# Optimization experiments

Hardware: AMD Instinct MI355X
Metric: run time of the kernel (lower is better)

Reference implementation:

```python
import jax, jax.numpy as jnp
import numpy as np

N_EMBD = 1024
BLOCK_SIZE = 2048
ATTN_SPAN = 256
LN_EPS = 1e-5


def _band_mask(T, span, dtype):
    ones = jnp.ones((T, T), dtype=dtype)
    # tril(.,0) * (1 - tril(.,-span)) -> causal band of width `span`
    return jnp.tril(ones, 0) * (1.0 - jnp.tril(ones, -span))


def setup_inputs() -> dict:
    key = jax.random.key(0)
    k_x, k_w, k_b, k_lw = jax.random.split(key, 4)
    B, T, C = 4, BLOCK_SIZE, N_EMBD
    x = jax.random.normal(k_x, (B, T, C), dtype=jnp.float32)
    # qkv_net: Linear(C, 3C) with bias (torch default)
    lim = 1.0 / np.sqrt(C)
    W_qkv = jax.random.uniform(k_w, (C, 3 * C), minval=-lim, maxval=lim, dtype=jnp.float32)
    b_qkv = jax.random.uniform(k_b, (3 * C,), minval=-lim, maxval=lim, dtype=jnp.float32)
    ln_w = jnp.ones((C,), dtype=jnp.float32)
    ln_b = jnp.zeros((C,), dtype=jnp.float32)
    return {"x": x, "W_qkv": W_qkv, "b_qkv": b_qkv, "ln_w": ln_w, "ln_b": ln_b}


def _layer_norm(h, w, b):
    mu = jnp.mean(h, axis=-1, keepdims=True)
    var = jnp.var(h, axis=-1, keepdims=True)
    return (h - mu) * jax.lax.rsqrt(var + LN_EPS) * w + b


def reference(x, W_qkv, b_qkv, ln_w, ln_b):
    B, T, C = x.shape
    qkv = x @ W_qkv + b_qkv  # [B,T,3C]
    q, k, v = jnp.split(qkv, 3, axis=-1)
    scale = np.sqrt(C * ATTN_SPAN).astype(np.float32)
    scores = jnp.einsum('bid,bjd->bij', q, k) / scale  # [B,T,T]
    scores = scores * _band_mask(T, ATTN_SPAN, x.dtype)[None, :, :]
    out = jnp.einsum('bij,bjd->bid', scores, v)  # [B,T,C]
    return _layer_norm(out, ln_w, ln_b)
```

## Files before the change

### kernel.cpp

```cpp
#include <hip/hip_runtime.h>
#include <cstdint>
#include <cstddef>

#define N_EMBD 1024
#define T_SEQ  2048
#define NBATCH 4
#define SPAN   256
#define C3     3072

typedef float  floatx4 __attribute__((ext_vector_type(4)));
typedef __bf16 bf16x8  __attribute__((ext_vector_type(8)));

__device__ inline unsigned short f2bf(float f) {
    union { float f; unsigned u; } x; x.f = f;
    unsigned u = x.u;
    unsigned r = (u + 0x7fffu + ((u >> 16) & 1u)) >> 16;
    return (unsigned short)r;
}

typedef __attribute__((address_space(1))) const void GVOID;
typedef __attribute__((address_space(3))) void LVOID;
__device__ inline void gl2lds16(const void* g, void* l) {
    __builtin_amdgcn_global_load_lds((GVOID*)g, (LVOID*)l, 16, 0, 0);
}

__global__ __launch_bounds__(256) void k_cvt_x(const float* __restrict__ x,
                                               unsigned short* __restrict__ xb) {
    int i = (blockIdx.x * 256 + threadIdx.x) * 4;
    float4 v = *(const float4*)(x + i);
    ushort4 o;
    o.x = f2bf(v.x); o.y = f2bf(v.y); o.z = f2bf(v.z); o.w = f2bf(v.w);
    *(ushort4*)(xb + i) = o;
}

__global__ __launch_bounds__(256) void k_cvt_w_t(const float* __restrict__ W,
                                                 unsigned short* __restrict__ WbT) {
    __shared__ unsigned short t[32][33];
    int tx = threadIdx.x & 31, ty = threadIdx.x >> 5;
    int k0 = blockIdx.x * 32, n0 = blockIdx.y * 32;
#pragma unroll
    for (int i = 0; i < 4; i++) {
        int k = k0 + ty + i * 8;
        t[ty + i * 8][tx] = f2bf(W[(size_t)k * C3 + n0 + tx]);
    }
    __syncthreads();
#pragma unroll
    for (int i = 0; i < 4; i++) {
        int n = n0 + ty + i * 8;
        WbT[(size_t)n * N_EMBD + k0 + tx] = t[tx][ty + i * 8];
    }
}

__global__ __launch_bounds__(256) void k_qkv_gemm(const unsigned short* __restrict__ Xb,
                                                  const unsigned short* __restrict__ WbT,
                                                  const float* __restrict__ bqkv,
                                                  unsigned short* __restrict__ qkv) {
    __shared__ unsigned short As[128 * 32];
    __shared__ unsigned short Bs[128 * 32];
    const int tid = threadIdx.x, lane = tid & 63, wave = tid >> 6;
    const int n0 = blockIdx.x * 128, m0 = blockIdx.y * 128;
    const int wr = wave >> 1, wc = wave & 1;

    floatx4 acc[4][4] = {};

    const int srow = wave * 16 + (lane >> 2);
    const int scol = (lane & 3) * 8;
    const unsigned short* gA = Xb  + (size_t)(m0 + srow) * N_EMBD + scol;
    const unsigned short* gB = WbT + (size_t)(n0 + srow) * N_EMBD + scol;

    for (int k0 = 0; k0 < N_EMBD; k0 += 32) {
        gl2lds16(gA + k0,              &As[(wave * 16) * 32]);
        gl2lds16(gA + 64 * N_EMBD + k0, &As[(64 + wave * 16) * 32]);
        gl2lds16(gB + k0,              &Bs[(wave * 16) * 32]);
        gl2lds16(gB + 64 * N_EMBD + k0, &Bs[(64 + wave * 16) * 32]);
        __syncthreads();

        bf16x8 a[4], b[4];
        const int qk = (lane >> 4) * 8;
        const int ra = wr * 64 + (lane & 15);
        const int rb = wc * 64 + (lane & 15);
#pragma unroll
        for (int mi = 0; mi < 4; mi++) a[mi] = *(const bf16x8*)&As[(ra + mi * 16) * 32 + qk];
#pragma unroll
        for (int ni = 0; ni < 4; ni++) b[ni] = *(const bf16x8*)&Bs[(rb + ni * 16) * 32 + qk];
#pragma unroll
        for (int mi = 0; mi < 4; mi++)
#pragma unroll
            for (int ni = 0; ni < 4; ni++)
                acc[mi][ni] = __builtin_amdgcn_mfma_f32_16x16x32_bf16(a[mi], b[ni], acc[mi][ni], 0, 0, 0);
        __syncthreads();
    }

    const int cn = lane & 15, q = lane >> 4;
#pragma unroll
    for (int ni = 0; ni < 4; ni++) {
        const int n = n0 + wc * 64 + ni * 16 + cn;
        const float bias = bqkv[n];
#pragma unroll
        for (int mi = 0; mi < 4; mi++) {
            const int mbase = m0 + wr * 64 + mi * 16 + q * 4;
#pragma unroll
            for (int r = 0; r < 4; r++)
                qkv[(size_t)(mbase + r) * C3 + n] = f2bf(acc[mi][ni][r] + bias);
        }
    }
}

__global__ __launch_bounds__(256) void k_v_t(const unsigned short* __restrict__ qkv,
                                             unsigned short* __restrict__ Vt) {
    __shared__ unsigned short t[32][33];
    int tx = threadIdx.x & 31, ty = threadIdx.x >> 5;
    int t0 = blockIdx.x * 32, c0 = blockIdx.y * 32, b = blockIdx.z;
#pragma unroll
    for (int i = 0; i < 4; i++) {
        int tt = t0 + ty + i * 8;
        t[ty + i * 8][tx] = qkv[(size_t)(b * T_SEQ + tt) * C3 + 2048 + c0 + tx];
    }
    __syncthreads();
#pragma unroll
    for (int i = 0; i < 4; i++) {
        int c = c0 + ty + i * 8;
        Vt[(size_t)b * N_EMBD * T_SEQ + (size_t)c * T_SEQ + t0 + tx] = t[tx][ty + i * 8];
    }
}

__global__ __launch_bounds__(256) void k_scores(const unsigned short* __restrict__ qkv,
                                                unsigned short* __restrict__ S) {
    const int jj = blockIdx.x, qb = blockIdx.y, b = blockIdx.z;
    const int jb = qb - 4 + jj;
    if (jb < 0) return;

    __shared__ unsigned short Qs[64 * 64];
    __shared__ unsigned short Ks[64 * 64];
    const int tid = threadIdx.x, lane = tid & 63, wave = tid >> 6;
    const int wr = wave >> 1, wc = wave & 1;

    floatx4 acc[2][2] = {};

    const int srow = wave * 8 + (lane >> 3);
    const int scol = (lane & 7) * 8;
    const unsigned short* gQ = qkv + (size_t)(b * T_SEQ + qb * 64 + srow) * C3 + scol;
    const unsigned short* gK = qkv + (size_t)(b * T_SEQ + jb * 64 + srow) * C3 + 1024 + scol;

    for (int k0 = 0; k0 < N_EMBD; k0 += 64) {
        gl2lds16(gQ + k0,                   &Qs[(wave * 8) * 64]);
        gl2lds16(gQ + (size_t)32 * C3 + k0, &Qs[(32 + wave * 8) * 64]);
        gl2lds16(gK + k0,                   &Ks[(wave * 8) * 64]);
        gl2lds16(gK + (size_t)32 * C3 + k0, &Ks[(32 + wave * 8) * 64]);
        __syncthreads();
#pragma unroll
        for (int ks = 0; ks < 2; ks++) {
            bf16x8 a[2], bb[2];
            const int qk = ks * 32 + (lane >> 4) * 8;
#pragma unroll
            for (int mi = 0; mi < 2; mi++) a[mi]  = *(const bf16x8*)&Qs[(wr * 32 + mi * 16 + (lane & 15)) * 64 + qk];
#pragma unroll
            for (int ni = 0; ni < 2; ni++) bb[ni] = *(const bf16x8*)&Ks[(wc * 32 + ni * 16 + (lane & 15)) * 64 + qk];
#pragma unroll
            for (int mi = 0; mi < 2; mi++)
#pragma unroll
                for (int ni = 0; ni < 2; ni++)
                    acc[mi][ni] = __builtin_amdgcn_mfma_f32_16x16x32_bf16(a[mi], bb[ni], acc[mi][ni], 0, 0, 0);
        }
        __syncthreads();
    }

    unsigned short* Sb = S + (((size_t)(b * 32 + qb) * 5 + jj) << 12);
    const int cn = lane & 15, q = lane >> 4;
#pragma unroll
    for (int mi = 0; mi < 2; mi++)
#pragma unroll
        for (int ni = 0; ni < 2; ni++)
#pragma unroll
            for (int r = 0; r < 4; r++) {
                const int il = wr * 32 + mi * 16 + q * 4 + r;
                const int jl = wc * 32 + ni * 16 + cn;
                const int gi = qb * 64 + il, gj = jb * 64 + jl;
                const float v = ((gj <= gi) && (gj > gi - 256)) ? acc[mi][ni][r] * (1.0f / 512.0f) : 0.0f;
                Sb[il * 64 + jl] = f2bf(v);
            }
}

__global__ __launch_bounds__(256) void k_sv(const unsigned short* __restrict__ S,
                                            const unsigned short* __restrict__ Vt,
                                            float* __restrict__ out) {
    const int cg = blockIdx.x, qb = blockIdx.y, b = blockIdx.z;
    const int c0 = cg * 128;

    __shared__ unsigned short Ss[64 * 64];
    __shared__ unsigned short Vs[128 * 64];
    const int tid = threadIdx.x, lane = tid & 63, wave = tid >> 6;
    const int wr = wave >> 1, wc = wave & 1;

    floatx4 acc[2][4] = {};

    const int srow = wave * 8 + (lane >> 3);
    const int scol = (lane & 7) * 8;

    for (int jj = 0; jj < 5; jj++) {
        const int jb = qb - 4 + jj;
        if (jb < 0) continue;

        const unsigned short* gS = S + (((size_t)(b * 32 + qb) * 5 + jj) << 12) + srow * 64 + scol;
        gl2lds16(gS,           &Ss[(wave * 8) * 64]);
        gl2lds16(gS + 32 * 64, &Ss[(32 + wave * 8) * 64]);
        const unsigned short* gV = Vt + (size_t)b * N_EMBD * T_SEQ
                                      + (size_t)(c0 + srow) * T_SEQ + jb * 64 + scol;
#pragma unroll
        for (int is = 0; is < 4; is++)
            gl2lds16(gV + (size_t)is * 32 * T_SEQ, &Vs[(is * 32 + wave * 8) * 64]);
        __syncthreads();
#pragma unroll
        for (int ks = 0; ks < 2; ks++) {
            bf16x8 a[2], bb[4];
            const int qk = ks * 32 + (lane >> 4) * 8;
#pragma unroll
            for (int mi = 0; mi < 2; mi++) a[mi]  = *(const bf16x8*)&Ss[(wr * 32 + mi * 16 + (lane & 15)) * 64 + qk];
#pragma unroll
            for (int ni = 0; ni < 4; ni++) bb[ni] = *(const bf16x8*)&Vs[(wc * 64 + ni * 16 + (lane & 15)) * 64 + qk];
#pragma unroll
            for (int mi = 0; mi < 2; mi++)
#pragma unroll
                for (int ni = 0; ni < 4; ni++)
                    acc[mi][ni] = __builtin_amdgcn_mfma_f32_16x16x32_bf16(a[mi], bb[ni], acc[mi][ni], 0, 0, 0);
        }
        __syncthreads();
    }

    const int cn = lane & 15, q = lane >> 4;
#pragma unroll
    for (int mi = 0; mi < 2; mi++)
#pragma unroll
        for (int ni = 0; ni < 4; ni++)
#pragma unroll
            for (int r = 0; r < 4; r++) {
                const int il = wr * 32 + mi * 16 + q * 4 + r;
                const int cl = wc * 64 + ni * 16 + cn;
                out[(size_t)(b * T_SEQ + qb * 64 + il) * N_EMBD + c0 + cl] = acc[mi][ni][r];
            }
}

__global__ __launch_bounds__(256) void k_ln(float* __restrict__ out,
                                            const float* __restrict__ w,
                                            const float* __restrict__ bias) {
    __shared__ float red[8];
    const int t = threadIdx.x;
    float* p = out + (size_t)blockIdx.x * N_EMBD;
    float4 v = ((const float4*)p)[t];
    float s  = v.x + v.y + v.z + v.w;
    float sq = v.x * v.x + v.y * v.y + v.z * v.z + v.w * v.w;
#pragma unroll
    for (int off = 32; off; off >>= 1) {
        s  += __shfl_down(s, off, 64);
        sq += __shfl_down(sq, off, 64);
    }
    const int wave = t >> 6, lane = t & 63;
    if (lane == 0) { red[wave] = s; red[4 + wave] = sq; }
    __syncthreads();
    const float ts = red[0] + red[1] + red[2] + red[3];
    const float tq = red[4] + red[5] + red[6] + red[7];
    const float mean = ts * (1.0f / N_EMBD);
    const float var  = tq * (1.0f / N_EMBD) - mean * mean;
    const float rs = rsqrtf(var + 1e-5f);
    float4 wv = ((const float4*)w)[t];
    float4 bv = ((const float4*)bias)[t];
    float4 o;
    o.x = (v.x - mean) * rs * wv.x + bv.x;
    o.y = (v.y - mean) * rs * wv.y + bv.y;
    o.z = (v.z - mean) * rs * wv.z + bv.z;
    o.w = (v.w - mean) * rs * wv.w + bv.w;
    ((float4*)p)[t] = o;
}

extern "C" void kernel_launch(void* const* d_in, const int* in_sizes, int n_in,
                              void* d_out, int out_size, void* d_ws, size_t ws_size,
                              hipStream_t stream) {
    const float* x  = (const float*)d_in[0];
    const float* W  = (const float*)d_in[1];
    const float* bq = (const float*)d_in[2];
    const float* lw = (const float*)d_in[3];
    const float* lb = (const float*)d_in[4];
    float* out = (float*)d_out;
    char* ws = (char*)d_ws;

    unsigned short* Xb   = (unsigned short*)(ws + 0);
    unsigned short* Sbuf = (unsigned short*)(ws + 0);
    unsigned short* WbT  = (unsigned short*)(ws + 16777216);
    unsigned short* qkv  = (unsigned short*)(ws + 23068672);
    unsigned short* Vt   = (unsigned short*)(ws + 73400320);

    k_cvt_x   <<<8192,            256, 0, stream>>>(x, Xb);
    k_cvt_w_t <<<dim3(32, 96),    256, 0, stream>>>(W, WbT);
    k_qkv_gemm<<<dim3(24, 64),    256, 0, stream>>>(Xb, WbT, bq, qkv);
    k_v_t     <<<dim3(64, 32, 4), 256, 0, stream>>>(qkv, Vt);
    k_scores  <<<dim3(5, 32, 4),  256, 0, stream>>>(qkv, Sbuf);
    k_sv      <<<dim3(8, 32, 4),  256, 0, stream>>>(Sbuf, Vt, out);
    k_ln      <<<8192,            256, 0, stream>>>(out, lw, lb);
}
```

Measured before the change: 213.5 us.

## Fuse conversion kernels, transpose V in GEMM epilogue, use 128-row attention tiles

The x and W bf16 conversions become a single launch. The V transpose moves into the QKV GEMM epilogue through an LDS staging tile, which removes the separate transpose kernel and the extra qkv round trip. Q and K are stored packed. The score and SV kernels switch from 64-row to 128-row tiles with 3 key blocks instead of 5, and LDS loads use an XOR-swizzled layout to avoid bank conflicts. This cuts launches, redundant band work and memory traffic, at the cost of fewer blocks in the attention kernels, which may lower occupancy.

```diff
diff --git a/kernel.cpp b/kernel.cpp
--- a/kernel.cpp
+++ b/kernel.cpp
@@ -24,61 +24,69 @@
     __builtin_amdgcn_global_load_lds((GVOID*)g, (LVOID*)l, 16, 0, 0);
 }
 
-__global__ __launch_bounds__(256) void k_cvt_x(const float* __restrict__ x,
-                                               unsigned short* __restrict__ xb) {
-    int i = (blockIdx.x * 256 + threadIdx.x) * 4;
-    float4 v = *(const float4*)(x + i);
-    ushort4 o;
-    o.x = f2bf(v.x); o.y = f2bf(v.y); o.z = f2bf(v.z); o.w = f2bf(v.w);
-    *(ushort4*)(xb + i) = o;
-}
-
-__global__ __launch_bounds__(256) void k_cvt_w_t(const float* __restrict__ W,
-                                                 unsigned short* __restrict__ WbT) {
+__device__ inline void stage128x32(const unsigned short* g, size_t stride,
+                                   unsigned short* lds, int lane, int wave) {
+    const int r     = wave * 16 + (lane >> 2);
+    const int chunk = (lane & 3) ^ ((lane >> 3) & 3);
+    const unsigned short* src = g + (size_t)r * stride + chunk * 8;
+    gl2lds16(src,               &lds[(wave * 16) * 32]);
+    gl2lds16(src + 64 * stride, &lds[(64 + wave * 16) * 32]);
+}
+
+__global__ __launch_bounds__(256) void k_prep(const float* __restrict__ x,
+                                              unsigned short* __restrict__ Xb,
+                                              const float* __restrict__ W,
+                                              unsigned short* __restrict__ WbT) {
     __shared__ unsigned short t[32][33];
-    int tx = threadIdx.x & 31, ty = threadIdx.x >> 5;
-    int k0 = blockIdx.x * 32, n0 = blockIdx.y * 32;
-#pragma unroll
-    for (int i = 0; i < 4; i++) {
-        int k = k0 + ty + i * 8;
-        t[ty + i * 8][tx] = f2bf(W[(size_t)k * C3 + n0 + tx]);
-    }
-    __syncthreads();
-#pragma unroll
-    for (int i = 0; i < 4; i++) {
-        int n = n0 + ty + i * 8;
-        WbT[(size_t)n * N_EMBD + k0 + tx] = t[tx][ty + i * 8];
+    if (blockIdx.x < 8192) {
+        int i = (blockIdx.x * 256 + threadIdx.x) * 4;
+        float4 v = *(const float4*)(x + i);
+        ushort4 o;
+        o.x = f2bf(v.x); o.y = f2bf(v.y); o.z = f2bf(v.z); o.w = f2bf(v.w);
+        *(ushort4*)(Xb + i) = o;
+    } else {
+        int bid = blockIdx.x - 8192;
+        int k0 = (bid & 31) * 32, n0 = (bid >> 5) * 32;
+        int tx = threadIdx.x & 31, ty = threadIdx.x >> 5;
+#pragma unroll
+        for (int i = 0; i < 4; i++) {
+            int k = k0 + ty + i * 8;
+            t[ty + i * 8][tx] = f2bf(W[(size_t)k * C3 + n0 + tx]);
+        }
+        __syncthreads();
+#pragma unroll
+        for (int i = 0; i < 4; i++) {
+            int n = n0 + ty + i * 8;
+            WbT[(size_t)n * N_EMBD + k0 + tx] = t[tx][ty + i * 8];
+        }
     }
 }
 
 __global__ __launch_bounds__(256) void k_qkv_gemm(const unsigned short* __restrict__ Xb,
                                                   const unsigned short* __restrict__ WbT,
                                                   const float* __restrict__ bqkv,
-                                                  unsigned short* __restrict__ qkv) {
-    __shared__ unsigned short As[128 * 32];
-    __shared__ unsigned short Bs[128 * 32];
+                                                  unsigned short* __restrict__ QK,
+                                                  unsigned short* __restrict__ Vt) {
+    __shared__ unsigned short smem[17408];
+    unsigned short* As = smem;
+    unsigned short* Bs = smem + 4096;
     const int tid = threadIdx.x, lane = tid & 63, wave = tid >> 6;
     const int n0 = blockIdx.x * 128, m0 = blockIdx.y * 128;
     const int wr = wave >> 1, wc = wave & 1;
 
     floatx4 acc[4][4] = {};
 
-    const int srow = wave * 16 + (lane >> 2);
-    const int scol = (lane & 3) * 8;
-    const unsigned short* gA = Xb  + (size_t)(m0 + srow) * N_EMBD + scol;
-    const unsigned short* gB = WbT + (size_t)(n0 + srow) * N_EMBD + scol;
+    const unsigned short* gA = Xb  + (size_t)m0 * N_EMBD;
+    const unsigned short* gB = WbT + (size_t)n0 * N_EMBD;
+    const int qk = ((lane >> 4) ^ ((lane >> 1) & 3)) * 8;
+    const int ra = wr * 64 + (lane & 15);
+    const int rb = wc * 64 + (lane & 15);
 
     for (int k0 = 0; k0 < N_EMBD; k0 += 32) {
-        gl2lds16(gA + k0,              &As[(wave * 16) * 32]);
-        gl2lds16(gA + 64 * N_EMBD + k0, &As[(64 + wave * 16) * 32]);
-        gl2lds16(gB + k0,              &Bs[(wave * 16) * 32]);
-        gl2lds16(gB + 64 * N_EMBD + k0, &Bs[(64 + wave * 16) * 32]);
-        __syncthreads();
-
+        stage128x32(gA + k0, N_EMBD, As, lane, wave);
+        stage128x32(gB + k0, N_EMBD, Bs, lane, wave);
+        __syncthreads();
         bf16x8 a[4], b[4];
-        const int qk = (lane >> 4) * 8;
-        const int ra = wr * 64 + (lane & 15);
-        const int rb = wc * 64 + (lane & 15);
 #pragma unroll
         for (int mi = 0; mi < 4; mi++) a[mi] = *(const bf16x8*)&As[(ra + mi * 16) * 32 + qk];
 #pragma unroll
@@ -92,92 +100,95 @@
     }
 
     const int cn = lane & 15, q = lane >> 4;
-#pragma unroll
-    for (int ni = 0; ni < 4; ni++) {
-        const int n = n0 + wc * 64 + ni * 16 + cn;
-        const float bias = bqkv[n];
-#pragma unroll
-        for (int mi = 0; mi < 4; mi++) {
-            const int mbase = m0 + wr * 64 + mi * 16 + q * 4;
-#pragma unroll
-            for (int r = 0; r < 4; r++)
-                qkv[(size_t)(mbase + r) * C3 + n] = f2bf(acc[mi][ni][r] + bias);
-        }
-    }
-}
-
-__global__ __launch_bounds__(256) void k_v_t(const unsigned short* __restrict__ qkv,
-                                             unsigned short* __restrict__ Vt) {
-    __shared__ unsigned short t[32][33];
-    int tx = threadIdx.x & 31, ty = threadIdx.x >> 5;
-    int t0 = blockIdx.x * 32, c0 = blockIdx.y * 32, b = blockIdx.z;
-#pragma unroll
-    for (int i = 0; i < 4; i++) {
-        int tt = t0 + ty + i * 8;
-        t[ty + i * 8][tx] = qkv[(size_t)(b * T_SEQ + tt) * C3 + 2048 + c0 + tx];
-    }
-    __syncthreads();
-#pragma unroll
-    for (int i = 0; i < 4; i++) {
-        int c = c0 + ty + i * 8;
-        Vt[(size_t)b * N_EMBD * T_SEQ + (size_t)c * T_SEQ + t0 + tx] = t[tx][ty + i * 8];
-    }
-}
-
-__global__ __launch_bounds__(256) void k_scores(const unsigned short* __restrict__ qkv,
+    if (n0 < 2048) {
+#pragma unroll
+        for (int ni = 0; ni < 4; ni++) {
+            const int n = n0 + wc * 64 + ni * 16 + cn;
+            const float bias = bqkv[n];
+#pragma unroll
+            for (int mi = 0; mi < 4; mi++) {
+                const int mbase = m0 + wr * 64 + mi * 16 + q * 4;
+#pragma unroll
+                for (int r = 0; r < 4; r++)
+                    QK[(size_t)(mbase + r) * 2048 + n] = f2bf(acc[mi][ni][r] + bias);
+            }
+        }
+    } else {
+        unsigned short* tp = smem;
+#pragma unroll
+        for (int ni = 0; ni < 4; ni++) {
+            const int cl = wc * 64 + ni * 16 + cn;
+            const float bias = bqkv[n0 + cl];
+#pragma unroll
+            for (int mi = 0; mi < 4; mi++) {
+                const int tl = wr * 64 + mi * 16 + q * 4;
+#pragma unroll
+                for (int r = 0; r < 4; r++)
+                    tp[cl * 136 + tl + r] = f2bf(acc[mi][ni][r] + bias);
+            }
+        }
+        __syncthreads();
+        const int clw = tid >> 1, half = tid & 1;
+        const int b = m0 >> 11, tg = (m0 & 2047) + half * 64;
+        const int cg = n0 - 2048 + clw;
+        unsigned short* dst = Vt + ((size_t)(b * 1024 + cg)) * 2048 + tg;
+        const unsigned short* src = tp + clw * 136 + half * 64;
+#pragma unroll
+        for (int i = 0; i < 8; i++)
+            *(uint4*)(dst + i * 8) = *(const uint4*)(src + i * 8);
+    }
+}
+
+__global__ __launch_bounds__(256) void k_scores(const unsigned short* __restrict__ QK,
                                                 unsigned short* __restrict__ S) {
     const int jj = blockIdx.x, qb = blockIdx.y, b = blockIdx.z;
-    const int jb = qb - 4 + jj;
+    const int jb = qb - 2 + jj;
     if (jb < 0) return;
 
-    __shared__ unsigned short Qs[64 * 64];
-    __shared__ unsigned short Ks[64 * 64];
+    __shared__ unsigned short smem[8192];
+    unsigned short* As = smem;
+    unsigned short* Bs = smem + 4096;
     const int tid = threadIdx.x, lane = tid & 63, wave = tid >> 6;
     const int wr = wave >> 1, wc = wave & 1;
 
-    floatx4 acc[2][2] = {};
-
-    const int srow = wave * 8 + (lane >> 3);
-    const int scol = (lane & 7) * 8;
-    const unsigned short* gQ = qkv + (size_t)(b * T_SEQ + qb * 64 + srow) * C3 + scol;
-    const unsigned short* gK = qkv + (size_t)(b * T_SEQ + jb * 64 + srow) * C3 + 1024 + scol;
-
-    for (int k0 = 0; k0 < N_EMBD; k0 += 64) {
-        gl2lds16(gQ + k0,                   &Qs[(wave * 8) * 64]);
-        gl2lds16(gQ + (size_t)32 * C3 + k0, &Qs[(32 + wave * 8) * 64]);
-        gl2lds16(gK + k0,                   &Ks[(wave * 8) * 64]);
-        gl2lds16(gK + (size_t)32 * C3 + k0, &Ks[(32 + wave * 8) * 64]);
-        __syncthreads();
-#pragma unroll
-        for (int ks = 0; ks < 2; ks++) {
-            bf16x8 a[2], bb[2];
-            const int qk = ks * 32 + (lane >> 4) * 8;
-#pragma unroll
-            for (int mi = 0; mi < 2; mi++) a[mi]  = *(const bf16x8*)&Qs[(wr * 32 + mi * 16 + (lane & 15)) * 64 + qk];
-#pragma unroll
-            for (int ni = 0; ni < 2; ni++) bb[ni] = *(const bf16x8*)&Ks[(wc * 32 + ni * 16 + (lane & 15)) * 64 + qk];
-#pragma unroll
-            for (int mi = 0; mi < 2; mi++)
-#pragma unroll
-                for (int ni = 0; ni < 2; ni++)
-                    acc[mi][ni] = __builtin_amdgcn_mfma_f32_16x16x32_bf16(a[mi], bb[ni], acc[mi][ni], 0, 0, 0);
-        }
-        __syncthreads();
-    }
-
-    unsigned short* Sb = S + (((size_t)(b * 32 + qb) * 5 + jj) << 12);
+    floatx4 acc[4][4] = {};
+
+    const unsigned short* gQ = QK + ((size_t)(b * T_SEQ + qb * 128)) * 2048;
+    const unsigned short* gK = QK + ((size_t)(b * T_SEQ + jb * 128)) * 2048 + 1024;
+    const int qk = ((lane >> 4) ^ ((lane >> 1) & 3)) * 8;
+    const int ra = wr * 64 + (lane & 15);
+    const int rb = wc * 64 + (lane & 15);
+
+    for (int k0 = 0; k0 < N_EMBD; k0 += 32) {
+        stage128x32(gQ + k0, 2048, As, lane, wave);
+        stage128x32(gK + k0, 2048, Bs, lane, wave);
+        __syncthreads();
+        bf16x8 a[4], bb[4];
+#pragma unroll
+        for (int mi = 0; mi < 4; mi++) a[mi]  = *(const bf16x8*)&As[(ra + mi * 16) * 32 + qk];
+#pragma unroll
+        for (int ni = 0; ni < 4; ni++) bb[ni] = *(const bf16x8*)&Bs[(rb + ni * 16) * 32 + qk];
+#pragma unroll
+        for (int mi = 0; mi < 4; mi++)
+#pragma unroll
+            for (int ni = 0; ni < 4; ni++)
+                acc[mi][ni] = __builtin_amdgcn_mfma_f32_16x16x32_bf16(a[mi], bb[ni], acc[mi][ni], 0, 0, 0);
+        __syncthreads();
+    }
+
+    unsigned short* Sb = S + ((size_t)(b * 16 + qb)) * (128 * 384);
     const int cn = lane & 15, q = lane >> 4;
 #pragma unroll
-    for (int mi = 0; mi < 2; mi++)
-#pragma unroll
-        for (int ni = 0; ni < 2; ni++)
+    for (int mi = 0; mi < 4; mi++)
+#pragma unroll
+        for (int ni = 0; ni < 4; ni++)
 #pragma unroll
             for (int r = 0; r < 4; r++) {
-                const int il = wr * 32 + mi * 16 + q * 4 + r;
-                const int jl = wc * 32 + ni * 16 + cn;
-                const int gi = qb * 64 + il, gj = jb * 64 + jl;
-                const float v = ((gj <= gi) && (gj > gi - 256)) ? acc[mi][ni][r] * (1.0f / 512.0f) : 0.0f;
-                Sb[il * 64 + jl] = f2bf(v);
+                const int il = wr * 64 + mi * 16 + q * 4 + r;
+                const int jl = wc * 64 + ni * 16 + cn;
+                const int gi = qb * 128 + il, gj = jb * 128 + jl;
+                const float v = ((gj <= gi) && (gj > gi - SPAN)) ? acc[mi][ni][r] * (1.0f / 512.0f) : 0.0f;
+                Sb[il * 384 + jj * 128 + jl] = f2bf(v);
             }
 }
 
@@ -187,56 +198,52 @@
     const int cg = blockIdx.x, qb = blockIdx.y, b = blockIdx.z;
     const int c0 = cg * 128;
 
-    __shared__ unsigned short Ss[64 * 64];
-    __shared__ unsigned short Vs[128 * 64];
+    __shared__ unsigned short smem[8192];
+    unsigned short* As = smem;
+    unsigned short* Bs = smem + 4096;
     const int tid = threadIdx.x, lane = tid & 63, wave = tid >> 6;
     const int wr = wave >> 1, wc = wave & 1;
 
-    floatx4 acc[2][4] = {};
-
-    const int srow = wave * 8 + (lane >> 3);
-    const int scol = (lane & 7) * 8;
-
-    for (int jj = 0; jj < 5; jj++) {
-        const int jb = qb - 4 + jj;
+    floatx4 acc[4][4] = {};
+
+    const unsigned short* Sb = S + ((size_t)(b * 16 + qb)) * (128 * 384);
+    const unsigned short* gV = Vt + ((size_t)(b * 1024 + c0)) * 2048;
+    const int qk = ((lane >> 4) ^ ((lane >> 1) & 3)) * 8;
+    const int ra = wr * 64 + (lane & 15);
+    const int rb = wc * 64 + (lane & 15);
+
+    for (int jj = 0; jj < 3; jj++) {
+        const int jb = qb - 2 + jj;
         if (jb < 0) continue;
-
-        const unsigned short* gS = S + (((size_t)(b * 32 + qb) * 5 + jj) << 12) + srow * 64 + scol;
-        gl2lds16(gS,           &Ss[(wave * 8) * 64]);
-        gl2lds16(gS + 32 * 64, &Ss[(32 + wave * 8) * 64]);
-        const unsigned short* gV = Vt + (size_t)b * N_EMBD * T_SEQ
-                                      + (size_t)(c0 + srow) * T_SEQ + jb * 64 + scol;
-#pragma unroll
-        for (int is = 0; is < 4; is++)
-            gl2lds16(gV + (size_t)is * 32 * T_SEQ, &Vs[(is * 32 + wave * 8) * 64]);
-        __syncthreads();
-#pragma unroll
-        for (int ks = 0; ks < 2; ks++) {
-            bf16x8 a[2], bb[4];
-            const int qk = ks * 32 + (lane >> 4) * 8;
-#pragma unroll
-            for (int mi = 0; mi < 2; mi++) a[mi]  = *(const bf16x8*)&Ss[(wr * 32 + mi * 16 + (lane & 15)) * 64 + qk];
-#pragma unroll
-            for (int ni = 0; ni < 4; ni++) bb[ni] = *(const bf16x8*)&Vs[(wc * 64 + ni * 16 + (lane & 15)) * 64 + qk];
-#pragma unroll
-            for (int mi = 0; mi < 2; mi++)
+#pragma unroll
+        for (int k0 = 0; k0 < 128; k0 += 32) {
+            stage128x32(Sb + jj * 128 + k0, 384, As, lane, wave);
+            stage128x32(gV + jb * 128 + k0, 2048, Bs, lane, wave);
+            __syncthreads();
+            bf16x8 a[4], bb[4];
+#pragma unroll
+            for (int mi = 0; mi < 4; mi++) a[mi]  = *(const bf16x8*)&As[(ra + mi * 16) * 32 + qk];
+#pragma unroll
+            for (int ni = 0; ni < 4; ni++) bb[ni] = *(const bf16x8*)&Bs[(rb + ni * 16) * 32 + qk];
+#pragma unroll
+            for (int mi = 0; mi < 4; mi++)
 #pragma unroll
                 for (int ni = 0; ni < 4; ni++)
                     acc[mi][ni] = __builtin_amdgcn_mfma_f32_16x16x32_bf16(a[mi], bb[ni], acc[mi][ni], 0, 0, 0);
-        }
-        __syncthreads();
+            __syncthreads();
+        }
     }
 
     const int cn = lane & 15, q = lane >> 4;
 #pragma unroll
-    for (int mi = 0; mi < 2; mi++)
+    for (int mi = 0; mi < 4; mi++)
 #pragma unroll
         for (int ni = 0; ni < 4; ni++)
 #pragma unroll
             for (int r = 0; r < 4; r++) {
-                const int il = wr * 32 + mi * 16 + q * 4 + r;
+                const int il = wr * 64 + mi * 16 + q * 4 + r;
                 const int cl = wc * 64 + ni * 16 + cn;
-                out[(size_t)(b * T_SEQ + qb * 64 + il) * N_EMBD + c0 + cl] = acc[mi][ni][r];
+                out[((size_t)(b * T_SEQ + qb * 128 + il)) * N_EMBD + c0 + cl] = acc[mi][ni][r];
             }
 }
 
@@ -286,14 +293,12 @@
     unsigned short* Xb   = (unsigned short*)(ws + 0);
     unsigned short* Sbuf = (unsigned short*)(ws + 0);
     unsigned short* WbT  = (unsigned short*)(ws + 16777216);
-    unsigned short* qkv  = (unsigned short*)(ws + 23068672);
-    unsigned short* Vt   = (unsigned short*)(ws + 73400320);
-
-    k_cvt_x   <<<8192,            256, 0, stream>>>(x, Xb);
-    k_cvt_w_t <<<dim3(32, 96),    256, 0, stream>>>(W, WbT);
-    k_qkv_gemm<<<dim3(24, 64),    256, 0, stream>>>(Xb, WbT, bq, qkv);
-    k_v_t     <<<dim3(64, 32, 4), 256, 0, stream>>>(qkv, Vt);
-    k_scores  <<<dim3(5, 32, 4),  256, 0, stream>>>(qkv, Sbuf);
-    k_sv      <<<dim3(8, 32, 4),  256, 0, stream>>>(Sbuf, Vt, out);
+    unsigned short* QK   = (unsigned short*)(ws + 23068672);
+    unsigned short* Vt   = (unsigned short*)(ws + 56623104);
+
+    k_prep    <<<11264,           256, 0, stream>>>(x, Xb, W, WbT);
+    k_qkv_gemm<<<dim3(24, 64),    256, 0, stream>>>(Xb, WbT, bq, QK, Vt);
+    k_scores  <<<dim3(3, 16, 4),  256, 0, stream>>>(QK, Sbuf);
+    k_sv      <<<dim3(8, 16, 4),  256, 0, stream>>>(Sbuf, Vt, out);
     k_ln      <<<8192,            256, 0, stream>>>(out, lw, lb);
 }
```

Result: slower. 222.6 us (+4.3%).
